# Kernel optimization log

Hardware: AMD Instinct MI355X
Metric: run time of the kernel (lower is better)

Reference implementation:

```python
import jax, jax.numpy as jnp
import numpy as np

B, H, W, C = 32, 64, 64, 512
NH, WH, WW = 16, 8, 8
SH, SW = 4, 4
FF = 2048
META = 384
A = WH * WW
EPS = 1e-5


def _rel_coords_log():
    # pairwise relative coords in log-space, shape (A*A, 2)
    coords = np.stack(np.meshgrid(np.arange(WH), np.arange(WW), indexing='ij')).reshape(2, -1)
    rel = coords[:, :, None] - coords[:, None, :]
    rel = rel.transpose(1, 2, 0).reshape(-1, 2).astype(np.float32)
    return np.sign(rel) * np.log1p(np.abs(rel))


def _attn_mask():
    # shifted-window attention mask, shape (nW, A, A)
    img = np.zeros((H, W), np.float32)
    cnt = 0
    for hs in (slice(0, -WH), slice(-WH, -SH), slice(-SH, None)):
        for ws in (slice(0, -WW), slice(-WW, -SW), slice(-SW, None)):
            img[hs, ws] = cnt
            cnt += 1
    mw = img.reshape(H // WH, WH, W // WW, WW).transpose(0, 2, 1, 3).reshape(-1, A)
    diff = mw[:, None, :] - mw[:, :, None]
    return np.where(diff != 0, -100.0, 0.0).astype(np.float32)


def setup_inputs():
    key = jax.random.key(0)
    ks = jax.random.split(key, 8)
    s = 0.02
    return {
        'x': jax.random.normal(ks[0], (B, H * W, C), jnp.float32),
        'qkv_w': jax.random.normal(ks[1], (C, 3 * C), jnp.float32) * s,
        'qkv_b': jnp.zeros((3 * C,), jnp.float32),
        'proj_w': jax.random.normal(ks[2], (C, C), jnp.float32) * s,
        'proj_b': jnp.zeros((C,), jnp.float32),
        'tau': jnp.ones((NH,), jnp.float32),
        'meta_w1': jax.random.normal(ks[3], (2, META), jnp.float32) * s,
        'meta_b1': jnp.zeros((META,), jnp.float32),
        'meta_w2': jax.random.normal(ks[4], (META, NH), jnp.float32) * s,
        'meta_b2': jnp.zeros((NH,), jnp.float32),
        'norm1_g': jnp.ones((C,), jnp.float32),
        'norm1_b': jnp.zeros((C,), jnp.float32),
        'norm2_g': jnp.ones((C,), jnp.float32),
        'norm2_b': jnp.zeros((C,), jnp.float32),
        'mlp_w1': jax.random.normal(ks[5], (C, FF), jnp.float32) * s,
        'mlp_b1': jnp.zeros((FF,), jnp.float32),
        'mlp_w2': jax.random.normal(ks[6], (FF, C), jnp.float32) * s,
        'mlp_b2': jnp.zeros((C,), jnp.float32),
    }


def _layernorm(x, g, b):
    mu = x.mean(-1, keepdims=True)
    var = ((x - mu) ** 2).mean(-1, keepdims=True)
    return (x - mu) * jax.lax.rsqrt(var + EPS) * g + b


def reference(x, qkv_w, qkv_b, proj_w, proj_b, tau, meta_w1, meta_b1, meta_w2, meta_b2,
              norm1_g, norm1_b, norm2_g, norm2_b, mlp_w1, mlp_b1, mlp_w2, mlp_b2):
    rel_log = jnp.asarray(_rel_coords_log())
    mask = jnp.asarray(_attn_mask())                 # (nW, A, A)
    nW = mask.shape[0]
    hd = C // NH

    # relative position bias from meta MLP (dropout inactive at eval)
    bias = jax.nn.relu(rel_log @ meta_w1 + meta_b1) @ meta_w2 + meta_b2  # (A*A, NH)
    bias = bias.T.reshape(NH, A, A)

    # cyclic shift + window partition
    xr = x.reshape(B, H, W, C)
    xr = jnp.roll(xr, (-SH, -SW), axis=(1, 2))
    xw = xr.reshape(B, H // WH, WH, W // WW, WW, C).transpose(0, 1, 3, 2, 4, 5)
    xw = xw.reshape(B * nW, A, C)

    qkv = (xw @ qkv_w + qkv_b).reshape(B * nW, A, 3, NH, hd).transpose(2, 0, 3, 1, 4)
    q, k, v = qkv[0], qkv[1], qkv[2]                 # (B*nW, NH, A, hd)

    qn = jnp.linalg.norm(q, axis=-1, keepdims=True)
    kn = jnp.linalg.norm(k, axis=-1, keepdims=True)
    denom = jnp.clip(qn * kn.transpose(0, 1, 3, 2), 1e-6, None)
    attn = jnp.einsum('wnid,wnjd->wnij', q, k) / denom
    attn = attn / jnp.clip(tau, 0.01, None).reshape(1, NH, 1, 1)
    attn = attn + bias[None]
    attn = attn.reshape(B, nW, NH, A, A) + mask[None, :, None]
    attn = jax.nn.softmax(attn.reshape(B * nW, NH, A, A), axis=-1)

    out = jnp.einsum('wnij,wnjd->wnid', attn, v)
    out = out.transpose(0, 2, 1, 3).reshape(B * nW, A, C)
    out = out @ proj_w + proj_b

    # window reverse + reverse shift
    out = out.reshape(B, H // WH, W // WW, WH, WW, C).transpose(0, 1, 3, 2, 4, 5).reshape(B, H, W, C)
    out = jnp.roll(out, (SH, SW), axis=(1, 2)).reshape(B, H * W, C)

    # swin-v2 post-norm residuals
    x = x + _layernorm(out, norm1_g, norm1_b)
    hmid = jax.nn.gelu(x @ mlp_w1 + mlp_b1, approximate=False) @ mlp_w2 + mlp_b2
    x = x + _layernorm(hmid, norm2_g, norm2_b)
    return x
```

## Files before the change

kernel.cpp:

```cpp
#include <hip/hip_runtime.h>

typedef unsigned short u16;
typedef __attribute__((ext_vector_type(8))) short     bf16x8;
typedef __attribute__((ext_vector_type(8))) unsigned short u16x8;
typedef __attribute__((ext_vector_type(4))) unsigned short u16x4;
typedef __attribute__((ext_vector_type(4))) float     f32x4;

#define GADDR(p) ((const __attribute__((address_space(1))) void*)(p))
#define LADDR(p) ((__attribute__((address_space(3))) void*)(p))

__device__ __forceinline__ u16 f2bf(float f) {
  unsigned u = __float_as_uint(f);
  u += 0x7fffu + ((u >> 16) & 1u);
  return (u16)(u >> 16);
}
__device__ __forceinline__ float bf2f(u16 h) {
  return __uint_as_float(((unsigned)h) << 16);
}

__global__ void wt_kernel(const float* __restrict__ w, u16* __restrict__ wt,
                          int K, int N) {
  size_t idx = (size_t)blockIdx.x * 256 + threadIdx.x;
  if (idx >= (size_t)K * N) return;
  int n = (int)(idx / K);
  int k = (int)(idx % K);
  wt[idx] = f2bf(w[(size_t)k * N + n]);
}

__global__ __launch_bounds__(64)
void bias_kernel(const float* __restrict__ w1, const float* __restrict__ b1,
                 const float* __restrict__ w2, const float* __restrict__ b2,
                 float* __restrict__ out) {
  const int p = blockIdx.x;
  const int i = p >> 6, j = p & 63;
  const float d0 = (float)((i >> 3) - (j >> 3));
  const float d1 = (float)((i & 7) - (j & 7));
  const float r0 = copysignf(log1pf(fabsf(d0)), d0);
  const float r1 = copysignf(log1pf(fabsf(d1)), d1);
  float part[16];
#pragma unroll
  for (int h = 0; h < 16; ++h) part[h] = 0.f;
  for (int m = threadIdx.x; m < 384; m += 64) {
    float hv = fmaxf(r0 * w1[m] + r1 * w1[384 + m] + b1[m], 0.f);
#pragma unroll
    for (int h = 0; h < 16; ++h) part[h] += hv * w2[m * 16 + h];
  }
#pragma unroll
  for (int h = 0; h < 16; ++h) {
    float v = part[h];
#pragma unroll
    for (int off = 32; off; off >>= 1) v += __shfl_xor(v, off);
    if (threadIdx.x == 0) out[(size_t)h * 4096 + p] = v + b2[h];
  }
}

__global__ __launch_bounds__(64)
void bias2_kernel(const float* __restrict__ bb, float* __restrict__ b2) {
  const int blk = blockIdx.x;
  const int h = blk >> 4, mi = (blk >> 2) & 3, ni = blk & 3;
  const int lane = threadIdx.x, fr = lane & 15, fq = lane >> 4;
  float4 o;
  o.x = bb[(size_t)h * 4096 + (mi * 16 + fq * 4 + 0) * 64 + ni * 16 + fr];
  o.y = bb[(size_t)h * 4096 + (mi * 16 + fq * 4 + 1) * 64 + ni * 16 + fr];
  o.z = bb[(size_t)h * 4096 + (mi * 16 + fq * 4 + 2) * 64 + ni * 16 + fr];
  o.w = bb[(size_t)h * 4096 + (mi * 16 + fq * 4 + 3) * 64 + ni * 16 + fr];
  ((float4*)b2)[(size_t)blk * 64 + lane] = o;
}

__global__ __launch_bounds__(128)
void partition_kernel(const float* __restrict__ x, u16* __restrict__ xw) {
  const size_t r = blockIdx.x;
  const int w   = (int)(r >> 6);
  const int i   = (int)(r & 63);
  const int b   = w >> 6;
  const int win = w & 63;
  const int hs = (((win >> 3) << 3) + (i >> 3) + 4) & 63;
  const int ws2 = (((win & 7) << 3) + (i & 7) + 4) & 63;
  const float4* src = (const float4*)(x + (((size_t)b << 12) + hs * 64 + ws2) * 512);
  u16* dst = xw + r * 512;
  const int t = threadIdx.x;
  float4 v = src[t];
  u16x4 o;
  o[0] = f2bf(v.x); o[1] = f2bf(v.y); o[2] = f2bf(v.z); o[3] = f2bf(v.w);
  *(u16x4*)(dst + t * 4) = o;
}

template <int MODE>
__global__ __launch_bounds__(512, 1)
void gemm8(const u16* __restrict__ A, const u16* __restrict__ Wt,
           const float* __restrict__ bias, void* __restrict__ outp,
           int M, int N, int K) {
  __shared__ u16 lds[65536];
  const int t = threadIdx.x;
  const int gx = gridDim.x;
  const int nwg = gx * gridDim.y;
  const int wg = blockIdx.y * gx + blockIdx.x;
  const int swzb = (wg & 7) * (nwg >> 3) + (wg >> 3);
  const int n0 = (swzb % gx) * 256;
  const int m0 = (swzb / gx) * 256;

  const int lane = t & 63;
  const int wid = t >> 6;
  const int wr = (wid >> 2) * 128;
  const int wc = (wid & 3) * 64;
  const int fr = lane & 15, fq = lane >> 4;
  const int c0 = (fq ^ (fr & 7)) * 8;
  const int c1 = ((4 + fq) ^ (fr & 7)) * 8;

  const int tq = t >> 3;
  const int scol = ((t & 7) ^ (tq & 7)) * 8;
  const u16* Asrc = A  + (size_t)(m0 + tq) * K + scol;
  const int rowB = (tq & 31) + ((t >> 8) << 6);
  const u16* Bsrc = Wt + (size_t)(n0 + rowB) * K + scol;
  const int dA = t * 8;
  const int dB = 16384 + ((t >> 8) << 11) + t * 8;

#define SG_A(tile, src, h) do {                                               \
    const int _d = ((tile) & 1) * 32768 + (h) * 4096 + dA;                    \
    const size_t _k = (size_t)(src) * 64 + (size_t)((h) * 64) * K;            \
    __builtin_amdgcn_global_load_lds(GADDR(Asrc + _k), LADDR(&lds[_d]), 16, 0, 0); \
    __builtin_amdgcn_global_load_lds(GADDR(Asrc + _k + (size_t)128 * K),      \
                                     LADDR(&lds[_d + 8192]), 16, 0, 0);       \
  } while (0)
#define SG_B(tile, src, h) do {                                               \
    const int _d = ((tile) & 1) * 32768 + (h) * 2048 + dB;                    \
    const size_t _k = (size_t)(src) * 64 + (size_t)((h) * 32) * K;            \
    __builtin_amdgcn_global_load_lds(GADDR(Bsrc + _k), LADDR(&lds[_d]), 16, 0, 0); \
    __builtin_amdgcn_global_load_lds(GADDR(Bsrc + _k + (size_t)128 * K),      \
                                     LADDR(&lds[_d + 8192]), 16, 0, 0);       \
  } while (0)

  f32x4 acc[8][4];
#pragma unroll
  for (int a = 0; a < 8; ++a)
#pragma unroll
    for (int b = 0; b < 4; ++b) acc[a][b] = (f32x4){0.f, 0.f, 0.f, 0.f};

  const int NT = K >> 6;
  SG_A(0, 0, 0); SG_A(0, 0, 1); SG_B(0, 0, 0); SG_B(0, 0, 1);
  SG_A(1, 1, 0); SG_B(1, 1, 0); SG_B(1, 1, 1);
  asm volatile("s_waitcnt vmcnt(6)" ::: "memory");
  __builtin_amdgcn_s_barrier();

  for (int s = 0; s < NT; ++s) {
    const int sb = (s & 1) << 15;
    const u16* la = lds + sb;
    const u16* lb = lds + sb + 16384;
    bf16x8 af[8], bf0[4], bf1[4];
#pragma unroll
    for (int mi = 0; mi < 4; ++mi) {
      const int r = (wr + mi * 16 + fr) * 64;
      af[mi * 2]     = *(const bf16x8*)&la[r + c0];
      af[mi * 2 + 1] = *(const bf16x8*)&la[r + c1];
    }
#pragma unroll
    for (int ni = 0; ni < 2; ++ni) {
      const int r = (wc + ni * 16 + fr) * 64;
      bf0[ni * 2]     = *(const bf16x8*)&lb[r + c0];
      bf0[ni * 2 + 1] = *(const bf16x8*)&lb[r + c1];
    }
    if (s + 1 < NT) SG_A(s + 1, s + 1, 1);
    __builtin_amdgcn_s_barrier();
    asm volatile("s_waitcnt lgkmcnt(0)" ::: "memory");
    __builtin_amdgcn_sched_barrier(0);
    __builtin_amdgcn_s_setprio(1);
#pragma unroll
    for (int mi = 0; mi < 4; ++mi)
#pragma unroll
      for (int ni = 0; ni < 2; ++ni) {
        acc[mi][ni] = __builtin_amdgcn_mfma_f32_16x16x32_bf16(
            af[mi * 2], bf0[ni * 2], acc[mi][ni], 0, 0, 0);
        acc[mi][ni] = __builtin_amdgcn_mfma_f32_16x16x32_bf16(
            af[mi * 2 + 1], bf0[ni * 2 + 1], acc[mi][ni], 0, 0, 0);
      }
    __builtin_amdgcn_s_setprio(0);
    __builtin_amdgcn_s_barrier();
#pragma unroll
    for (int ni = 0; ni < 2; ++ni) {
      const int r = (wc + 32 + ni * 16 + fr) * 64;
      bf1[ni * 2]     = *(const bf16x8*)&lb[r + c0];
      bf1[ni * 2 + 1] = *(const bf16x8*)&lb[r + c1];
    }
    if (s + 2 < NT) SG_A(s + 2, s + 2, 0);
    __builtin_amdgcn_s_barrier();
    asm volatile("s_waitcnt lgkmcnt(0)" ::: "memory");
    __builtin_amdgcn_sched_barrier(0);
    __builtin_amdgcn_s_setprio(1);
#pragma unroll
    for (int mi = 0; mi < 4; ++mi)
#pragma unroll
      for (int ni = 0; ni < 2; ++ni) {
        acc[mi][2 + ni] = __builtin_amdgcn_mfma_f32_16x16x32_bf16(
            af[mi * 2], bf1[ni * 2], acc[mi][2 + ni], 0, 0, 0);
        acc[mi][2 + ni] = __builtin_amdgcn_mfma_f32_16x16x32_bf16(
            af[mi * 2 + 1], bf1[ni * 2 + 1], acc[mi][2 + ni], 0, 0, 0);
      }
    __builtin_amdgcn_s_setprio(0);
    __builtin_amdgcn_s_barrier();
#pragma unroll
    for (int mi = 0; mi < 4; ++mi) {
      const int r = (wr + 64 + mi * 16 + fr) * 64;
      af[mi * 2]     = *(const bf16x8*)&la[r + c0];
      af[mi * 2 + 1] = *(const bf16x8*)&la[r + c1];
    }
    if (s + 2 < NT) SG_B(s + 2, s + 2, 0);
    __builtin_amdgcn_s_barrier();
    asm volatile("s_waitcnt lgkmcnt(0)" ::: "memory");
    __builtin_amdgcn_sched_barrier(0);
    __builtin_amdgcn_s_setprio(1);
#pragma unroll
    for (int mi = 0; mi < 4; ++mi)
#pragma unroll
      for (int ni = 0; ni < 2; ++ni) {
        acc[4 + mi][ni] = __builtin_amdgcn_mfma_f32_16x16x32_bf16(
            af[mi * 2], bf0[ni * 2], acc[4 + mi][ni], 0, 0, 0);
        acc[4 + mi][ni] = __builtin_amdgcn_mfma_f32_16x16x32_bf16(
            af[mi * 2 + 1], bf0[ni * 2 + 1], acc[4 + mi][ni], 0, 0, 0);
      }
    __builtin_amdgcn_s_setprio(0);
    __builtin_amdgcn_s_barrier();
    if (s + 2 < NT) SG_B(s + 2, s + 2, 1);
    __builtin_amdgcn_s_barrier();
    __builtin_amdgcn_s_setprio(1);
#pragma unroll
    for (int mi = 0; mi < 4; ++mi)
#pragma unroll
      for (int ni = 0; ni < 2; ++ni) {
        acc[4 + mi][2 + ni] = __builtin_amdgcn_mfma_f32_16x16x32_bf16(
            af[mi * 2], bf1[ni * 2], acc[4 + mi][2 + ni], 0, 0, 0);
        acc[4 + mi][2 + ni] = __builtin_amdgcn_mfma_f32_16x16x32_bf16(
            af[mi * 2 + 1], bf1[ni * 2 + 1], acc[4 + mi][2 + ni], 0, 0, 0);
      }
    __builtin_amdgcn_s_setprio(0);
    if (s + 2 < NT) asm volatile("s_waitcnt vmcnt(6)" ::: "memory");
    else            asm volatile("s_waitcnt vmcnt(0)" ::: "memory");
    __builtin_amdgcn_s_barrier();
  }
#undef SG_A
#undef SG_B
  asm volatile("s_waitcnt vmcnt(0)" ::: "memory");
  __syncthreads();

  float bv4[4];
#pragma unroll
  for (int ni = 0; ni < 4; ++ni) bv4[ni] = bias[n0 + wc + ni * 16 + fr];

  u16* uW = &lds[wid * 8192];
  u16* og = (u16*)outp;
#pragma unroll
  for (int mi = 0; mi < 8; ++mi) {
#pragma unroll
    for (int ni = 0; ni < 4; ++ni)
#pragma unroll
      for (int j = 0; j < 4; ++j) {
        float v = acc[mi][ni][j] + bv4[ni];
        if (MODE == 2) {
          const float a2 = v * (1.5957691216f + 0.0713548162f * v * v);
          const float e = __expf(a2);
          v = v * (e * __builtin_amdgcn_rcpf(e + 1.0f));
        }
        uW[(fq * 4 + j) * 64 + ((ni ^ j ^ fq) & 3) * 16 + fr] = f2bf(v);
      }
#pragma unroll
    for (int p = 0; p < 2; ++p) {
      const int r = p * 8 + (lane >> 3);
      const int sg = (((lane & 7) >> 1) ^ (r & 3) ^ ((r >> 2) & 3)) & 3;
      u16x8 v8 = *(const u16x8*)&uW[r * 64 + sg * 16 + (lane & 1) * 8];
      const int row = m0 + wr + mi * 16 + r;
      *(u16x8*)&og[(size_t)row * N + n0 + wc + (lane & 7) * 8] = v8;
    }
  }
}

template <int LNM>
__global__ __launch_bounds__(512, 2)
void gemm_ln(const u16* __restrict__ A, const u16* __restrict__ Wt,
             const float* __restrict__ bias, const float* __restrict__ resid,
             const float* __restrict__ g, const float* __restrict__ bt,
             float* __restrict__ out1, u16* __restrict__ out1b, int K) {
  __shared__ u16 lds[40960];
  const int t = threadIdx.x;
  const int nwg = gridDim.x;
  const int wg = blockIdx.x;
  const int swz = (wg & 7) * (nwg >> 3) + (wg >> 3);
  const int m0 = swz * 128;

  const int lane = t & 63;
  const int wid = t >> 6;
  const int wc = wid * 64;
  const int fr = lane & 15, fq = lane >> 4;
  const int rx = (fr >> 1) & 3;

  const int srow = t >> 2;
  const int schk = ((t & 3) ^ ((srow >> 1) & 3)) * 8;
  const u16* Ag = A  + (size_t)(m0 + srow) * K + schk;
  const u16* Bg = Wt + (size_t)srow * K + schk;

#define GLSTAGE_A(tile, buf)                                                  \
    __builtin_amdgcn_global_load_lds(GADDR(Ag + (size_t)(tile) * 32),         \
        LADDR(&lds[(buf) * 20480 + t * 8]), 16, 0, 0)
#define GLSTAGE_B(tile, buf, p)                                               \
    __builtin_amdgcn_global_load_lds(                                         \
        GADDR(Bg + (size_t)(p) * 128 * K + (size_t)(tile) * 32),              \
        LADDR(&lds[(buf) * 20480 + 4096 + (p) * 4096 + t * 8]), 16, 0, 0)

  f32x4 acc[8][4];
#pragma unroll
  for (int a = 0; a < 8; ++a)
#pragma unroll
    for (int b = 0; b < 4; ++b) acc[a][b] = (f32x4){0.f, 0.f, 0.f, 0.f};

  const int NT = K >> 5;
  GLSTAGE_A(0, 0);
  GLSTAGE_B(0, 0, 0); GLSTAGE_B(0, 0, 1); GLSTAGE_B(0, 0, 2); GLSTAGE_B(0, 0, 3);
  asm volatile("s_waitcnt vmcnt(0)" ::: "memory");
  __builtin_amdgcn_s_barrier();

  for (int u = 0; u < NT; ++u) {
    const int cur = u & 1;
    const int stg = cur ^ 1;
    const u16* lb = lds + cur * 20480;
    bf16x8 bfr[4], af0[4], af1[4];
#pragma unroll
    for (int ni = 0; ni < 4; ++ni)
      bfr[ni] = *(const bf16x8*)&lb[4096 + (wc + ni * 16 + fr) * 32 + (fq ^ rx) * 8];
#pragma unroll
    for (int mi = 0; mi < 4; ++mi)
      af0[mi] = *(const bf16x8*)&lb[(mi * 16 + fr) * 32 + (fq ^ rx) * 8];
    if (u + 1 < NT) {
      GLSTAGE_A(u + 1, stg);
      GLSTAGE_B(u + 1, stg, 0); GLSTAGE_B(u + 1, stg, 1);
    }
    __builtin_amdgcn_s_barrier();
    asm volatile("s_waitcnt lgkmcnt(0)" ::: "memory");
    __builtin_amdgcn_sched_barrier(0);
    __builtin_amdgcn_s_setprio(1);
#pragma unroll
    for (int mi = 0; mi < 4; ++mi)
#pragma unroll
      for (int ni = 0; ni < 4; ++ni)
        acc[mi][ni] = __builtin_amdgcn_mfma_f32_16x16x32_bf16(
            af0[mi], bfr[ni], acc[mi][ni], 0, 0, 0);
    __builtin_amdgcn_s_setprio(0);
    __builtin_amdgcn_s_barrier();
#pragma unroll
    for (int mi = 0; mi < 4; ++mi)
      af1[mi] = *(const bf16x8*)&lb[((4 + mi) * 16 + fr) * 32 + (fq ^ rx) * 8];
    if (u + 1 < NT) {
      GLSTAGE_B(u + 1, stg, 2); GLSTAGE_B(u + 1, stg, 3);
    }
    __builtin_amdgcn_s_barrier();
    asm volatile("s_waitcnt lgkmcnt(0)" ::: "memory");
    __builtin_amdgcn_sched_barrier(0);
    __builtin_amdgcn_s_setprio(1);
#pragma unroll
    for (int mi = 0; mi < 4; ++mi)
#pragma unroll
      for (int ni = 0; ni < 4; ++ni)
        acc[4 + mi][ni] = __builtin_amdgcn_mfma_f32_16x16x32_bf16(
            af1[mi], bfr[ni], acc[4 + mi][ni], 0, 0, 0);
    __builtin_amdgcn_s_setprio(0);
    asm volatile("s_waitcnt vmcnt(0)" ::: "memory");
    __builtin_amdgcn_s_barrier();
  }
#undef GLSTAGE_A
#undef GLSTAGE_B

  __syncthreads();
  float bv4[4];
#pragma unroll
  for (int ni = 0; ni < 4; ++ni) bv4[ni] = bias[wc + ni * 16 + fr];
  float4 ga = ((const float4*)g)[lane * 2];
  float4 gb = ((const float4*)g)[lane * 2 + 1];
  float4 ba = ((const float4*)bt)[lane * 2];
  float4 bb = ((const float4*)bt)[lane * 2 + 1];
  const float gv[8] = {ga.x, ga.y, ga.z, ga.w, gb.x, gb.y, gb.z, gb.w};
  const float bv[8] = {ba.x, ba.y, ba.z, ba.w, bb.x, bb.y, bb.z, bb.w};
  float* fLN = (float*)lds;

#pragma unroll
  for (int mi = 0; mi < 8; ++mi) {
#pragma unroll
    for (int ni = 0; ni < 4; ++ni)
#pragma unroll
      for (int j = 0; j < 4; ++j) {
        const int ch = ((wid * 4 + ni) ^ (j << 2) ^ fq) & 31;
        fLN[(fq * 4 + j) * 512 + ch * 16 + fr] = acc[mi][ni][j] + bv4[ni];
      }
    __syncthreads();
#pragma unroll
    for (int rr = 0; rr < 2; ++rr) {
      const int r = wid * 2 + rr;
      const int gci = lane >> 1;
      const int ch = (gci ^ ((r & 3) << 2) ^ (r >> 2)) & 31;
      const int base = r * 512 + ch * 16 + (lane & 1) * 8;
      f32x4 va = *(const f32x4*)&fLN[base];
      f32x4 vb = *(const f32x4*)&fLN[base + 4];
      float v[8] = {va[0], va[1], va[2], va[3], vb[0], vb[1], vb[2], vb[3]};
      float s = 0.f, s2 = 0.f;
#pragma unroll
      for (int e = 0; e < 8; ++e) { s += v[e]; s2 = fmaf(v[e], v[e], s2); }
#pragma unroll
      for (int off = 32; off; off >>= 1) {
        s += __shfl_xor(s, off); s2 += __shfl_xor(s2, off);
      }
      const float mu = s * (1.f / 512.f);
      const float rs = rsqrtf(s2 * (1.f / 512.f) - mu * mu + 1e-5f);
      const int rowg = m0 + mi * 16 + r;
      size_t token;
      if (LNM == 0) {
        const int w = rowg >> 6, i = rowg & 63;
        const int b = w >> 6, win = w & 63;
        const int hs = (((win >> 3) << 3) + (i >> 3) + 4) & 63;
        const int ws2 = (((win & 7) << 3) + (i & 7) + 4) & 63;
        token = ((size_t)b << 12) + hs * 64 + ws2;
      } else {
        token = (size_t)rowg;
      }
      const float* rp = resid + token * 512 + lane * 8;
      float4 r0 = ((const float4*)rp)[0];
      float4 r1 = ((const float4*)rp)[1];
      const float rv[8] = {r0.x, r0.y, r0.z, r0.w, r1.x, r1.y, r1.z, r1.w};
      float o[8];
      u16x8 ob;
#pragma unroll
      for (int e = 0; e < 8; ++e) {
        o[e] = rv[e] + (v[e] - mu) * rs * gv[e] + bv[e];
        ob[e] = f2bf(o[e]);
      }
      float* op = out1 + token * 512 + lane * 8;
      ((f32x4*)op)[0] = (f32x4){o[0], o[1], o[2], o[3]};
      ((f32x4*)op)[1] = (f32x4){o[4], o[5], o[6], o[7]};
      if (LNM == 0) *(u16x8*)(out1b + token * 512 + lane * 8) = ob;
    }
    __syncthreads();
  }
}

__global__ __launch_bounds__(64)
void attn_kernel(const u16* __restrict__ qkv, const float* __restrict__ bias2,
                 const float* __restrict__ tau, u16* __restrict__ ao) {
  const int h = blockIdx.x;
  const int w = blockIdx.y;
  const int lane = threadIdx.x;
  const int fr = lane & 15, fq = lane >> 4;

  __shared__ u16 sh[7424];

  const size_t rowb = ((size_t)w * 64 + lane) * 1536 + (size_t)h * 32;
  u16x8 q8[4], k8[4], v8[4];
#pragma unroll
  for (int u = 0; u < 4; ++u) {
    q8[u] = ((const u16x8*)(qkv + rowb))[u];
    k8[u] = ((const u16x8*)(qkv + rowb + 512))[u];
    v8[u] = ((const u16x8*)(qkv + rowb + 1024))[u];
  }
  float qv[32], kv[32];
  float qn = 0.f, kn = 0.f;
#pragma unroll
  for (int d = 0; d < 32; ++d) {
    qv[d] = bf2f(q8[d >> 3][d & 7]); qn = fmaf(qv[d], qv[d], qn);
    kv[d] = bf2f(k8[d >> 3][d & 7]); kn = fmaf(kv[d], kv[d], kn);
  }
  const float itau = 1.0f / fmaxf(tau[h], 0.01f);
  const float qs = rsqrtf(fmaxf(qn, 1e-24f)) * itau;
  const float ks = rsqrtf(fmaxf(kn, 1e-24f));
#pragma unroll
  for (int u = 0; u < 4; ++u) {
    u16x8 qo, ko;
#pragma unroll
    for (int e = 0; e < 8; ++e) {
      qo[e] = f2bf(qv[u * 8 + e] * qs);
      ko[e] = f2bf(kv[u * 8 + e] * ks);
    }
    *(u16x8*)&sh[lane * 40 + u * 8] = qo;
    *(u16x8*)&sh[2560 + lane * 40 + u * 8] = ko;
  }
#pragma unroll
  for (int d = 0; d < 32; ++d)
    sh[5120 + d * 72 + lane] = v8[d >> 3][d & 7];
  __syncthreads();

  f32x4 acc[4][4];
  const float4* b2 = (const float4*)bias2 + (size_t)h * 1024 + lane;
#pragma unroll
  for (int mi = 0; mi < 4; ++mi)
#pragma unroll
    for (int ni = 0; ni < 4; ++ni) {
      float4 bv = b2[(mi * 4 + ni) * 64];
      acc[mi][ni] = (f32x4){bv.x, bv.y, bv.z, bv.w};
    }
  const int win = w & 63, wh = win >> 3, ww = win & 7;
  if (wh == 7 || ww == 7) {
    int labc[4];
#pragma unroll
    for (int ni = 0; ni < 4; ++ni) {
      const int c = ni * 16 + fr;
      labc[ni] = ((wh == 7) ? (((c >> 3) < 4) ? 1 : 2) : 0) * 3
               + ((ww == 7) ? (((c & 7) < 4) ? 1 : 2) : 0);
    }
#pragma unroll
    for (int mi = 0; mi < 4; ++mi)
#pragma unroll
      for (int j = 0; j < 4; ++j) {
        const int r = mi * 16 + fq * 4 + j;
        const int lr = ((wh == 7) ? (((r >> 3) < 4) ? 1 : 2) : 0) * 3
                     + ((ww == 7) ? (((r & 7) < 4) ? 1 : 2) : 0);
#pragma unroll
        for (int ni = 0; ni < 4; ++ni)
          if (lr != labc[ni]) acc[mi][ni][j] -= 100.f;
      }
  }

  {
    bf16x8 af[4], bf[4];
#pragma unroll
    for (int mi = 0; mi < 4; ++mi)
      af[mi] = *(const bf16x8*)&sh[(mi * 16 + fr) * 40 + fq * 8];
#pragma unroll
    for (int ni = 0; ni < 4; ++ni)
      bf[ni] = *(const bf16x8*)&sh[2560 + (ni * 16 + fr) * 40 + fq * 8];
#pragma unroll
    for (int mi = 0; mi < 4; ++mi)
#pragma unroll
      for (int ni = 0; ni < 4; ++ni)
        acc[mi][ni] = __builtin_amdgcn_mfma_f32_16x16x32_bf16(
            af[mi], bf[ni], acc[mi][ni], 0, 0, 0);
  }

  float lrec[4][4];
#pragma unroll
  for (int mi = 0; mi < 4; ++mi) {
#pragma unroll
    for (int j = 0; j < 4; ++j) {
      float m4 = fmaxf(fmaxf(acc[mi][0][j], acc[mi][1][j]),
                       fmaxf(acc[mi][2][j], acc[mi][3][j]));
#pragma unroll
      for (int mk = 1; mk < 16; mk <<= 1) m4 = fmaxf(m4, __shfl_xor(m4, mk));
      float e0 = __expf(acc[mi][0][j] - m4);
      float e1 = __expf(acc[mi][1][j] - m4);
      float e2 = __expf(acc[mi][2][j] - m4);
      float e3 = __expf(acc[mi][3][j] - m4);
      float s4 = (e0 + e1) + (e2 + e3);
#pragma unroll
      for (int mk = 1; mk < 16; mk <<= 1) s4 += __shfl_xor(s4, mk);
      lrec[mi][j] = __builtin_amdgcn_rcpf(s4);
      const int r = mi * 16 + fq * 4 + j;
      sh[r * 72 +  0 + fr] = f2bf(e0);
      sh[r * 72 + 16 + fr] = f2bf(e1);
      sh[r * 72 + 32 + fr] = f2bf(e2);
      sh[r * 72 + 48 + fr] = f2bf(e3);
    }
  }
  __syncthreads();

  f32x4 acc2[4][2];
#pragma unroll
  for (int mi = 0; mi < 4; ++mi)
#pragma unroll
    for (int n2 = 0; n2 < 2; ++n2) acc2[mi][n2] = (f32x4){0.f, 0.f, 0.f, 0.f};
#pragma unroll
  for (int kk = 0; kk < 2; ++kk) {
    bf16x8 pf[4], vf[2];
#pragma unroll
    for (int mi = 0; mi < 4; ++mi)
      pf[mi] = *(const bf16x8*)&sh[(mi * 16 + fr) * 72 + kk * 32 + fq * 8];
#pragma unroll
    for (int n2 = 0; n2 < 2; ++n2)
      vf[n2] = *(const bf16x8*)&sh[5120 + (n2 * 16 + fr) * 72 + kk * 32 + fq * 8];
#pragma unroll
    for (int mi = 0; mi < 4; ++mi)
#pragma unroll
      for (int n2 = 0; n2 < 2; ++n2)
        acc2[mi][n2] = __builtin_amdgcn_mfma_f32_16x16x32_bf16(
            pf[mi], vf[n2], acc2[mi][n2], 0, 0, 0);
  }

  u16* op = ao + ((size_t)w * 64) * 512 + (size_t)h * 32;
#pragma unroll
  for (int mi = 0; mi < 4; ++mi)
#pragma unroll
    for (int j = 0; j < 4; ++j) {
      const int r = mi * 16 + fq * 4 + j;
      const float sc = lrec[mi][j];
      op[(size_t)r * 512 +  0 + fr] = f2bf(acc2[mi][0][j] * sc);
      op[(size_t)r * 512 + 16 + fr] = f2bf(acc2[mi][1][j] * sc);
    }
}

extern "C" void kernel_launch(void* const* d_in, const int* in_sizes, int n_in,
                              void* d_out, int out_size, void* d_ws, size_t ws_size,
                              hipStream_t stream) {
  const float* x      = (const float*)d_in[0];
  const float* qkv_w  = (const float*)d_in[1];
  const float* qkv_b  = (const float*)d_in[2];
  const float* proj_w = (const float*)d_in[3];
  const float* proj_b = (const float*)d_in[4];
  const float* tau    = (const float*)d_in[5];
  const float* mw1    = (const float*)d_in[6];
  const float* mb1    = (const float*)d_in[7];
  const float* mw2    = (const float*)d_in[8];
  const float* mb2    = (const float*)d_in[9];
  const float* n1g    = (const float*)d_in[10];
  const float* n1b    = (const float*)d_in[11];
  const float* n2g    = (const float*)d_in[12];
  const float* n2b    = (const float*)d_in[13];
  const float* mlp_w1 = (const float*)d_in[14];
  const float* mlp_b1 = (const float*)d_in[15];
  const float* mlp_w2 = (const float*)d_in[16];
  const float* mlp_b2 = (const float*)d_in[17];

  char* ws = (char*)d_ws;
  u16*   WQKVT  = (u16*)  (ws + 0);
  u16*   WPROJT = (u16*)  (ws + 1572864);
  u16*   WM1T   = (u16*)  (ws + 2097152);
  u16*   WM2T   = (u16*)  (ws + 4194304);
  float* BIASB  = (float*)(ws + 6291456);
  float* BIAS2  = (float*)(ws + 6553600);
  const size_t CH0 = 8388608;

  int CB = 32;
  while (CB > 1 && CH0 + (size_t)CB * 33554432ull > ws_size) CB >>= 1;
  const int NCH = 32 / CB;
  const size_t Mc = (size_t)CB * 4096;

  u16*   XW   = (u16*)  (ws + CH0);
  u16*   QKV  = (u16*)  (ws + CH0 + Mc * 1024);
  u16*   HBUF = QKV;
  float* X1   = (float*)(ws + CH0 + Mc * 5120);
  u16*   X1B  = (u16*)  (ws + CH0 + Mc * 7168);
  u16*   AO   = XW;

  wt_kernel<<<(512 * 1536 + 255) / 256, 256, 0, stream>>>(qkv_w, WQKVT, 512, 1536);
  wt_kernel<<<(512 * 512 + 255) / 256, 256, 0, stream>>>(proj_w, WPROJT, 512, 512);
  wt_kernel<<<(512 * 2048 + 255) / 256, 256, 0, stream>>>(mlp_w1, WM1T, 512, 2048);
  wt_kernel<<<(2048 * 512 + 255) / 256, 256, 0, stream>>>(mlp_w2, WM2T, 2048, 512);
  bias_kernel<<<4096, 64, 0, stream>>>(mw1, mb1, mw2, mb2, BIASB);
  bias2_kernel<<<256, 64, 0, stream>>>(BIASB, BIAS2);

  const unsigned MB = (unsigned)(Mc / 256);
  const unsigned LB = (unsigned)(Mc / 128);

  for (int c = 0; c < NCH; ++c) {
    const float* xc = x + (size_t)c * Mc * 512;
    float* oc = (float*)d_out + (size_t)c * Mc * 512;

    partition_kernel<<<(unsigned)Mc, 128, 0, stream>>>(xc, XW);
    gemm8<0><<<dim3(6, MB), 512, 0, stream>>>(XW, WQKVT, qkv_b, QKV,
                                              (int)Mc, 1536, 512);
    attn_kernel<<<dim3(16, CB * 64), 64, 0, stream>>>(QKV, BIAS2, tau, AO);
    gemm_ln<0><<<LB, 512, 0, stream>>>(AO, WPROJT, proj_b, xc, n1g, n1b,
                                       X1, X1B, 512);
    gemm8<2><<<dim3(8, MB), 512, 0, stream>>>(X1B, WM1T, mlp_b1, HBUF,
                                              (int)Mc, 2048, 512);
    gemm_ln<1><<<LB, 512, 0, stream>>>(HBUF, WM2T, mlp_b2, X1, n2g, n2b,
                                       oc, nullptr, 2048);
  }
}
```

Baseline: 1.549 ms.

## Retile fused GEMM+LayerNorm to 64-row blocks with 4 waves

The fused GEMM+LayerNorm kernel moves from 128-row tiles with 8 waves (each covering 64 columns) to 64-row tiles with 4 waves (each covering 128 columns, 4x8 MFMA fragments). The K-loop pipeline is simplified from two half-phases with several barriers to one global-to-LDS staging per iteration followed by a single wait and barrier. The goal is twice as many workgroups for better CU occupancy and fewer barriers per K step. In exchange the B tile is reloaded once per 64 rows instead of 128, doubling weight traffic, and the simpler pipeline may expose more load latency.

```diff
diff --git a/kernel.cpp b/kernel.cpp
--- a/kernel.cpp
+++ b/kernel.cpp
@@ -273,21 +273,21 @@
 }
 
 template <int LNM>
-__global__ __launch_bounds__(512, 2)
+__global__ __launch_bounds__(256, 2)
 void gemm_ln(const u16* __restrict__ A, const u16* __restrict__ Wt,
              const float* __restrict__ bias, const float* __restrict__ resid,
              const float* __restrict__ g, const float* __restrict__ bt,
              float* __restrict__ out1, u16* __restrict__ out1b, int K) {
-  __shared__ u16 lds[40960];
+  __shared__ u16 lds[36864];
   const int t = threadIdx.x;
   const int nwg = gridDim.x;
   const int wg = blockIdx.x;
   const int swz = (wg & 7) * (nwg >> 3) + (wg >> 3);
-  const int m0 = swz * 128;
+  const int m0 = swz * 64;
 
   const int lane = t & 63;
   const int wid = t >> 6;
-  const int wc = wid * 64;
+  const int wc = wid * 128;
   const int fr = lane & 15, fq = lane >> 4;
   const int rx = (fr >> 1) & 3;
 
@@ -296,80 +296,59 @@
   const u16* Ag = A  + (size_t)(m0 + srow) * K + schk;
   const u16* Bg = Wt + (size_t)srow * K + schk;
 
-#define GLSTAGE_A(tile, buf)                                                  \
-    __builtin_amdgcn_global_load_lds(GADDR(Ag + (size_t)(tile) * 32),         \
-        LADDR(&lds[(buf) * 20480 + t * 8]), 16, 0, 0)
-#define GLSTAGE_B(tile, buf, p)                                               \
-    __builtin_amdgcn_global_load_lds(                                         \
-        GADDR(Bg + (size_t)(p) * 128 * K + (size_t)(tile) * 32),              \
-        LADDR(&lds[(buf) * 20480 + 4096 + (p) * 4096 + t * 8]), 16, 0, 0)
-
-  f32x4 acc[8][4];
-#pragma unroll
-  for (int a = 0; a < 8; ++a)
-#pragma unroll
-    for (int b = 0; b < 4; ++b) acc[a][b] = (f32x4){0.f, 0.f, 0.f, 0.f};
+#define LNSTAGE(tile, buf) do {                                               \
+    const int _b = (buf) * 18432;                                             \
+    const size_t _k = (size_t)(tile) * 32;                                    \
+    __builtin_amdgcn_global_load_lds(GADDR(Ag + _k), LADDR(&lds[_b + t * 8]), \
+                                     16, 0, 0);                               \
+    _Pragma("unroll")                                                         \
+    for (int _p = 0; _p < 8; ++_p)                                            \
+      __builtin_amdgcn_global_load_lds(                                       \
+          GADDR(Bg + (size_t)_p * 64 * K + _k),                               \
+          LADDR(&lds[_b + 2048 + _p * 2048 + t * 8]), 16, 0, 0);              \
+  } while (0)
+
+  f32x4 acc[4][8];
+#pragma unroll
+  for (int a = 0; a < 4; ++a)
+#pragma unroll
+    for (int b = 0; b < 8; ++b) acc[a][b] = (f32x4){0.f, 0.f, 0.f, 0.f};
 
   const int NT = K >> 5;
-  GLSTAGE_A(0, 0);
-  GLSTAGE_B(0, 0, 0); GLSTAGE_B(0, 0, 1); GLSTAGE_B(0, 0, 2); GLSTAGE_B(0, 0, 3);
+  LNSTAGE(0, 0);
   asm volatile("s_waitcnt vmcnt(0)" ::: "memory");
   __builtin_amdgcn_s_barrier();
 
   for (int u = 0; u < NT; ++u) {
     const int cur = u & 1;
-    const int stg = cur ^ 1;
-    const u16* lb = lds + cur * 20480;
-    bf16x8 bfr[4], af0[4], af1[4];
-#pragma unroll
-    for (int ni = 0; ni < 4; ++ni)
-      bfr[ni] = *(const bf16x8*)&lb[4096 + (wc + ni * 16 + fr) * 32 + (fq ^ rx) * 8];
-#pragma unroll
-    for (int mi = 0; mi < 4; ++mi)
-      af0[mi] = *(const bf16x8*)&lb[(mi * 16 + fr) * 32 + (fq ^ rx) * 8];
+    const u16* lb = lds + cur * 18432;
+    bf16x8 af[4], bfr[8];
+#pragma unroll
+    for (int mi = 0; mi < 4; ++mi)
+      af[mi] = *(const bf16x8*)&lb[(mi * 16 + fr) * 32 + (fq ^ rx) * 8];
+#pragma unroll
+    for (int ni = 0; ni < 8; ++ni)
+      bfr[ni] = *(const bf16x8*)&lb[2048 + (wc + ni * 16 + fr) * 32 + (fq ^ rx) * 8];
+    if (u + 1 < NT) LNSTAGE(u + 1, cur ^ 1);
+    __builtin_amdgcn_s_setprio(1);
+#pragma unroll
+    for (int mi = 0; mi < 4; ++mi)
+#pragma unroll
+      for (int ni = 0; ni < 8; ++ni)
+        acc[mi][ni] = __builtin_amdgcn_mfma_f32_16x16x32_bf16(
+            af[mi], bfr[ni], acc[mi][ni], 0, 0, 0);
+    __builtin_amdgcn_s_setprio(0);
     if (u + 1 < NT) {
-      GLSTAGE_A(u + 1, stg);
-      GLSTAGE_B(u + 1, stg, 0); GLSTAGE_B(u + 1, stg, 1);
-    }
-    __builtin_amdgcn_s_barrier();
-    asm volatile("s_waitcnt lgkmcnt(0)" ::: "memory");
-    __builtin_amdgcn_sched_barrier(0);
-    __builtin_amdgcn_s_setprio(1);
-#pragma unroll
-    for (int mi = 0; mi < 4; ++mi)
-#pragma unroll
-      for (int ni = 0; ni < 4; ++ni)
-        acc[mi][ni] = __builtin_amdgcn_mfma_f32_16x16x32_bf16(
-            af0[mi], bfr[ni], acc[mi][ni], 0, 0, 0);
-    __builtin_amdgcn_s_setprio(0);
-    __builtin_amdgcn_s_barrier();
-#pragma unroll
-    for (int mi = 0; mi < 4; ++mi)
-      af1[mi] = *(const bf16x8*)&lb[((4 + mi) * 16 + fr) * 32 + (fq ^ rx) * 8];
-    if (u + 1 < NT) {
-      GLSTAGE_B(u + 1, stg, 2); GLSTAGE_B(u + 1, stg, 3);
-    }
-    __builtin_amdgcn_s_barrier();
-    asm volatile("s_waitcnt lgkmcnt(0)" ::: "memory");
-    __builtin_amdgcn_sched_barrier(0);
-    __builtin_amdgcn_s_setprio(1);
-#pragma unroll
-    for (int mi = 0; mi < 4; ++mi)
-#pragma unroll
-      for (int ni = 0; ni < 4; ++ni)
-        acc[4 + mi][ni] = __builtin_amdgcn_mfma_f32_16x16x32_bf16(
-            af1[mi], bfr[ni], acc[4 + mi][ni], 0, 0, 0);
-    __builtin_amdgcn_s_setprio(0);
-    asm volatile("s_waitcnt vmcnt(0)" ::: "memory");
-    __builtin_amdgcn_s_barrier();
-  }
-#undef GLSTAGE_A
-#undef GLSTAGE_B
+      asm volatile("s_waitcnt vmcnt(0)" ::: "memory");
+      __builtin_amdgcn_s_barrier();
+    }
+  }
+#undef LNSTAGE
 
   __syncthreads();
-  float bv4[4];
-#pragma unroll
-  for (int ni = 0; ni < 4; ++ni) bv4[ni] = bias[wc + ni * 16 + fr];
+  float bv8[8];
+#pragma unroll
+  for (int ni = 0; ni < 8; ++ni) bv8[ni] = bias[wc + ni * 16 + fr];
   float4 ga = ((const float4*)g)[lane * 2];
   float4 gb = ((const float4*)g)[lane * 2 + 1];
   float4 ba = ((const float4*)bt)[lane * 2];
@@ -379,20 +358,20 @@
   float* fLN = (float*)lds;
 
 #pragma unroll
-  for (int mi = 0; mi < 8; ++mi) {
-#pragma unroll
-    for (int ni = 0; ni < 4; ++ni)
+  for (int mi = 0; mi < 4; ++mi) {
+#pragma unroll
+    for (int ni = 0; ni < 8; ++ni)
 #pragma unroll
       for (int j = 0; j < 4; ++j) {
-        const int ch = ((wid * 4 + ni) ^ (j << 2) ^ fq) & 31;
-        fLN[(fq * 4 + j) * 512 + ch * 16 + fr] = acc[mi][ni][j] + bv4[ni];
+        const int ch = ((wid * 8 + ni) ^ (j << 2) ^ fq) & 31;
+        fLN[(fq * 4 + j) * 512 + ch * 16 + fr] = acc[mi][ni][j] + bv8[ni];
       }
     __syncthreads();
 #pragma unroll
-    for (int rr = 0; rr < 2; ++rr) {
-      const int r = wid * 2 + rr;
+    for (int rr = 0; rr < 4; ++rr) {
+      const int r = wid * 4 + rr;
       const int gci = lane >> 1;
-      const int ch = (gci ^ ((r & 3) << 2) ^ (r >> 2)) & 31;
+      const int ch = (gci ^ ((r & 3) << 2) ^ ((r >> 2) & 3)) & 31;
       const int base = r * 512 + ch * 16 + (lane & 1) * 8;
       f32x4 va = *(const f32x4*)&fLN[base];
       f32x4 vb = *(const f32x4*)&fLN[base + 4];
@@ -638,8 +617,8 @@
   bias_kernel<<<4096, 64, 0, stream>>>(mw1, mb1, mw2, mb2, BIASB);
   bias2_kernel<<<256, 64, 0, stream>>>(BIASB, BIAS2);
 
-  const unsigned MB = (unsigned)(Mc / 256);
-  const unsigned LB = (unsigned)(Mc / 128);
+  const unsigned MB  = (unsigned)(Mc / 256);
+  const unsigned LB2 = (unsigned)(Mc / 64);
 
   for (int c = 0; c < NCH; ++c) {
     const float* xc = x + (size_t)c * Mc * 512;
@@ -649,11 +628,11 @@
     gemm8<0><<<dim3(6, MB), 512, 0, stream>>>(XW, WQKVT, qkv_b, QKV,
                                               (int)Mc, 1536, 512);
     attn_kernel<<<dim3(16, CB * 64), 64, 0, stream>>>(QKV, BIAS2, tau, AO);
-    gemm_ln<0><<<LB, 512, 0, stream>>>(AO, WPROJT, proj_b, xc, n1g, n1b,
-                                       X1, X1B, 512);
+    gemm_ln<0><<<LB2, 256, 0, stream>>>(AO, WPROJT, proj_b, xc, n1g, n1b,
+                                        X1, X1B, 512);
     gemm8<2><<<dim3(8, MB), 512, 0, stream>>>(X1B, WM1T, mlp_b1, HBUF,
                                               (int)Mc, 2048, 512);
-    gemm_ln<1><<<LB, 512, 0, stream>>>(HBUF, WM2T, mlp_b2, X1, n2g, n2b,
-                                       oc, nullptr, 2048);
-  }
-}
+    gemm_ln<1><<<LB2, 256, 0, stream>>>(HBUF, WM2T, mlp_b2, X1, n2g, n2b,
+                                        oc, nullptr, 2048);
+  }
+}
```

After: 1.605 ms. 1.04x slower.
